# Optimization experiments

Hardware: AMD Instinct MI355X
Metric: run time of the kernel (lower is better)

The kernel has to match this reference:

```python
import jax, jax.numpy as jnp
import numpy as np

PNUM = 128
BATCH = 8192


def setup_inputs() -> dict:
    key = jax.random.key(0)
    k0, k1, k2 = jax.random.split(key, 3)
    return {
        "pred0": jax.random.normal(k0, (BATCH, PNUM, 2), dtype=jnp.float32),
        "pred1": jax.random.normal(k1, (BATCH, PNUM, 2), dtype=jnp.float32),
        "gt": jax.random.normal(k2, (BATCH, PNUM, 2), dtype=jnp.float32),
    }


def _smooth_l1(d):
    # F.smooth_l1_loss with default beta=1.0, reduction='none'
    a = jnp.abs(d)
    return jnp.where(a < 1.0, 0.5 * d * d, a - 0.5)


def _match_loss(pred, gt):
    # pred, gt: [B, pnum, 2]
    pnum = pred.shape[1]
    # cyclic index: idx[i, j] = (i + j) % pnum  (row i = gt rolled by i)
    idx = (jnp.arange(pnum)[:, None] + jnp.arange(pnum)[None, :]) % pnum
    gt_expand = gt[:, idx]                      # [B, pnum, pnum, 2]
    diff = pred[:, None, :, :] - gt_expand      # broadcast pred over shift dim i
    dis = _smooth_l1(diff).sum(-1).mean(axis=2)  # [B, pnum] mean over vertices j
    return jnp.min(dis, axis=1)                  # min over cyclic shift i -> [B]


def reference(pred0, pred1, gt):
    loss = _match_loss(pred0, gt).mean() + _match_loss(pred1, gt).mean()
    return loss / 2.0
```

## Files before the change

### kernel.cpp

```cpp
#include <hip/hip_runtime.h>

#define PNUM 128
#define BATCH 8192
#define WPB 4
#define GRID1 (BATCH / (2 * WPB))

typedef _Float16 h2 __attribute__((ext_vector_type(2)));
typedef _Float16 h4 __attribute__((ext_vector_type(4)));
typedef _Float16 h8 __attribute__((ext_vector_type(8)));

__device__ __forceinline__ h2 cvt2(float x, float y) {
    return __builtin_bit_cast(h2, __builtin_amdgcn_cvt_pkrtz(x, y));
}
__device__ __forceinline__ h4 cvt4(float4 v) {
    h2 a = cvt2(v.x, v.y), b = cvt2(v.z, v.w);
    return (h4){a.x, a.y, b.x, b.y};
}

__device__ __forceinline__ void unit(h2 p, h2 q, float& acc) {
    h2 d = p - q;
    h2 a = __builtin_bit_cast(h2, __builtin_bit_cast(unsigned, d) & 0x7fff7fffu);
    h2 m = __builtin_elementwise_min(a, (h2)(_Float16)1.0f);
    h2 t = __builtin_elementwise_fma(m, (h2)(_Float16)-0.5f, a);
    acc = __builtin_amdgcn_fdot2(m, t, acc, false);
}

__device__ __forceinline__ h2 lo2(h4 v) { return __builtin_shufflevector(v, v, 0, 1); }
__device__ __forceinline__ h2 hi2(h4 v) { return __builtin_shufflevector(v, v, 2, 3); }
__device__ __forceinline__ h4 lo4(h8 v) { return __builtin_shufflevector(v, v, 0, 1, 2, 3); }
__device__ __forceinline__ h4 hi4(h8 v) { return __builtin_shufflevector(v, v, 4, 5, 6, 7); }
__device__ __forceinline__ h2 el2(h8 v, int i) {
    return (h2){v[2 * i], v[2 * i + 1]};
}

__global__ __launch_bounds__(64 * WPB, 4) void match_fused(
        const float* __restrict__ pred0,
        const float* __restrict__ pred1,
        const float* __restrict__ gt,
        float* __restrict__ out) {
    __shared__ __align__(16) h4 ring [WPB][2][128];
    __shared__ __align__(16) h4 preds[WPB][2][2][64];

    const int t  = threadIdx.x;
    const int k  = t & 63;
    const int w  = __builtin_amdgcn_readfirstlane(t >> 6);
    const int h  = k >> 5;
    const int kk = k & 31;
    const int b  = 2 * (blockIdx.x * WPB + w) + h;

    h4* ring4 = ring[w][h];
    h4* q0 = preds[w][h][0];
    h4* q1 = preds[w][h][1];

    const float4* gv4 = (const float4*)(gt    + (size_t)b * (PNUM * 2));
    const float4* p0v = (const float4*)(pred0 + (size_t)b * (PNUM * 2));
    const float4* p1v = (const float4*)(pred1 + (size_t)b * (PNUM * 2));
    {
        h4 v = cvt4(gv4[kk]);      ring4[kk]      = v; ring4[kk + 64] = v;
        v    = cvt4(gv4[kk + 32]); ring4[kk + 32] = v; ring4[kk + 96] = v;
        q0[kk]      = cvt4(p0v[kk]);
        q0[kk + 32] = cvt4(p0v[kk + 32]);
        q1[kk]      = cvt4(p1v[kk]);
        q1[kk + 32] = cvt4(p1v[kk + 32]);
    }

    const h8* q0_8 = (const h8*)q0;
    const h8* q1_8 = (const h8*)q1;

    h8 wi = *(const h8*)&ring4[2 * kk];
    h4 w0 = lo4(wi), w1 = hi4(wi);

    float r00 = 0.f, r01 = 0.f, r02 = 0.f, r03 = 0.f;
    float r10 = 0.f, r11 = 0.f, r12 = 0.f, r13 = 0.f;

#pragma unroll 4
    for (int hh = 0; hh < 32; ++hh) {
        h8 n  = *(const h8*)&ring4[2 * kk + 2 * hh + 2];
        h8 P0 = q0_8[hh];
        h8 P1 = q1_8[hh];
        h4 w2 = lo4(n), w3 = hi4(n);

        h2 A0 = lo2(w0), A1 = hi2(w0), A2 = lo2(w1), A3 = hi2(w1);
        h2 A4 = lo2(w2), A5 = hi2(w2), A6 = lo2(w3);
        h2 p0a = el2(P0, 0), p0b = el2(P0, 1), p0c = el2(P0, 2), p0d = el2(P0, 3);
        h2 p1a = el2(P1, 0), p1b = el2(P1, 1), p1c = el2(P1, 2), p1d = el2(P1, 3);

        unit(p0a, A0, r00); unit(p0b, A1, r00); unit(p0c, A2, r00); unit(p0d, A3, r00);
        unit(p0a, A1, r01); unit(p0b, A2, r01); unit(p0c, A3, r01); unit(p0d, A4, r01);
        unit(p0a, A2, r02); unit(p0b, A3, r02); unit(p0c, A4, r02); unit(p0d, A5, r02);
        unit(p0a, A3, r03); unit(p0b, A4, r03); unit(p0c, A5, r03); unit(p0d, A6, r03);

        unit(p1a, A0, r10); unit(p1b, A1, r10); unit(p1c, A2, r10); unit(p1d, A3, r10);
        unit(p1a, A1, r11); unit(p1b, A2, r11); unit(p1c, A3, r11); unit(p1d, A4, r11);
        unit(p1a, A2, r12); unit(p1b, A3, r12); unit(p1c, A4, r12); unit(p1d, A5, r12);
        unit(p1a, A3, r13); unit(p1b, A4, r13); unit(p1c, A5, r13); unit(p1d, A6, r13);

        w0 = w2; w1 = w3;
    }

    float m0 = fminf(fminf(r00, r01), fminf(r02, r03));
    float m1 = fminf(fminf(r10, r11), fminf(r12, r13));
#pragma unroll
    for (int m = 16; m > 0; m >>= 1) {
        m0 = fminf(m0, __shfl_xor(m0, m, 64));
        m1 = fminf(m1, __shfl_xor(m1, m, 64));
    }
    float s = m0 + m1;
    s += __shfl_xor(s, 32, 64);

    __shared__ float bsum[WPB];
    if (k == 0) bsum[w] = s;
    __syncthreads();
    if (t == 0) {
        float blockpart = bsum[0] + bsum[1] + bsum[2] + bsum[3];
        atomicAdd(out, blockpart * (1.0f / (2.0f * BATCH * PNUM)));
    }
}

extern "C" void kernel_launch(void* const* d_in, const int* in_sizes, int n_in,
                              void* d_out, int out_size, void* d_ws, size_t ws_size,
                              hipStream_t stream) {
    const float* pred0 = (const float*)d_in[0];
    const float* pred1 = (const float*)d_in[1];
    const float* gt    = (const float*)d_in[2];
    float* out = (float*)d_out;

    (void)hipMemsetAsync(out, 0, sizeof(float), stream);
    match_fused<<<GRID1, 64 * WPB, 0, stream>>>(pred0, pred1, gt, out);
}
```

Measured before the change: 116.6 us.

## Split vertex loop across wave pairs and merge partial shift sums in LDS

```diff
diff --git a/kernel.cpp b/kernel.cpp
--- a/kernel.cpp
+++ b/kernel.cpp
@@ -2,8 +2,7 @@
 
 #define PNUM 128
 #define BATCH 8192
-#define WPB 4
-#define GRID1 (BATCH / (2 * WPB))
+#define GRID1 (BATCH / 4)
 
 typedef _Float16 h2 __attribute__((ext_vector_type(2)));
 typedef _Float16 h4 __attribute__((ext_vector_type(4)));
@@ -29,28 +28,30 @@
 __device__ __forceinline__ h2 hi2(h4 v) { return __builtin_shufflevector(v, v, 2, 3); }
 __device__ __forceinline__ h4 lo4(h8 v) { return __builtin_shufflevector(v, v, 0, 1, 2, 3); }
 __device__ __forceinline__ h4 hi4(h8 v) { return __builtin_shufflevector(v, v, 4, 5, 6, 7); }
-__device__ __forceinline__ h2 el2(h8 v, int i) {
-    return (h2){v[2 * i], v[2 * i + 1]};
-}
+__device__ __forceinline__ h2 el2(h8 v, int i) { return (h2){v[2 * i], v[2 * i + 1]}; }
 
-__global__ __launch_bounds__(64 * WPB, 4) void match_fused(
+__global__ __launch_bounds__(256, 8) void match_fused(
         const float* __restrict__ pred0,
         const float* __restrict__ pred1,
         const float* __restrict__ gt,
         float* __restrict__ out) {
-    __shared__ __align__(16) h4 ring [WPB][2][128];
-    __shared__ __align__(16) h4 preds[WPB][2][2][64];
+    __shared__ __align__(16) h4 ring [4][128];
+    __shared__ __align__(16) h4 preds[4][2][64];
+    __shared__ float part[2][8][64];
 
-    const int t  = threadIdx.x;
-    const int k  = t & 63;
-    const int w  = __builtin_amdgcn_readfirstlane(t >> 6);
-    const int h  = k >> 5;
-    const int kk = k & 31;
-    const int b  = 2 * (blockIdx.x * WPB + w) + h;
+    const int t    = threadIdx.x;
+    const int k    = t & 63;
+    const int w    = __builtin_amdgcn_readfirstlane(t >> 6);
+    const int pair = w >> 1;
+    const int sK   = w & 1;
+    const int h    = k >> 5;
+    const int kk   = k & 31;
+    const int bb   = 2 * pair + h;
+    const int b    = blockIdx.x * 4 + bb;
 
-    h4* ring4 = ring[w][h];
-    h4* q0 = preds[w][h][0];
-    h4* q1 = preds[w][h][1];
+    h4* ring4 = ring[bb];
+    h4* q0 = preds[bb][0];
+    h4* q1 = preds[bb][1];
 
     const float4* gv4 = (const float4*)(gt    + (size_t)b * (PNUM * 2));
     const float4* p0v = (const float4*)(pred0 + (size_t)b * (PNUM * 2));
@@ -67,14 +68,15 @@
     const h8* q0_8 = (const h8*)q0;
     const h8* q1_8 = (const h8*)q1;
 
-    h8 wi = *(const h8*)&ring4[2 * kk];
+    const int h0 = 16 * sK;
+    h8 wi = *(const h8*)&ring4[2 * kk + 32 * sK];
     h4 w0 = lo4(wi), w1 = hi4(wi);
 
     float r00 = 0.f, r01 = 0.f, r02 = 0.f, r03 = 0.f;
     float r10 = 0.f, r11 = 0.f, r12 = 0.f, r13 = 0.f;
 
 #pragma unroll 4
-    for (int hh = 0; hh < 32; ++hh) {
+    for (int hh = h0; hh < h0 + 16; ++hh) {
         h8 n  = *(const h8*)&ring4[2 * kk + 2 * hh + 2];
         h8 P0 = q0_8[hh];
         h8 P1 = q1_8[hh];
@@ -98,22 +100,35 @@
         w0 = w2; w1 = w3;
     }
 
-    float m0 = fminf(fminf(r00, r01), fminf(r02, r03));
-    float m1 = fminf(fminf(r10, r11), fminf(r12, r13));
+    if (sK) {
+        float* pp = &part[pair][0][k];
+        pp[0]       = r00; pp[64]      = r01; pp[2 * 64] = r02; pp[3 * 64] = r03;
+        pp[4 * 64]  = r10; pp[5 * 64]  = r11; pp[6 * 64] = r12; pp[7 * 64] = r13;
+    }
+    __syncthreads();
+
+    float s2 = 0.f;
+    if (!sK) {
+        const float* pp = &part[pair][0][k];
+        r00 += pp[0];       r01 += pp[64];      r02 += pp[2 * 64]; r03 += pp[3 * 64];
+        r10 += pp[4 * 64];  r11 += pp[5 * 64];  r12 += pp[6 * 64]; r13 += pp[7 * 64];
+
+        float m0 = fminf(fminf(r00, r01), fminf(r02, r03));
+        float m1 = fminf(fminf(r10, r11), fminf(r12, r13));
 #pragma unroll
-    for (int m = 16; m > 0; m >>= 1) {
-        m0 = fminf(m0, __shfl_xor(m0, m, 64));
-        m1 = fminf(m1, __shfl_xor(m1, m, 64));
+        for (int m = 16; m > 0; m >>= 1) {
+            m0 = fminf(m0, __shfl_xor(m0, m, 64));
+            m1 = fminf(m1, __shfl_xor(m1, m, 64));
+        }
+        s2 = m0 + m1;
+        s2 += __shfl_xor(s2, 32, 64);
     }
-    float s = m0 + m1;
-    s += __shfl_xor(s, 32, 64);
 
-    __shared__ float bsum[WPB];
-    if (k == 0) bsum[w] = s;
+    __shared__ float bsum[2];
+    if (!sK && k == 0) bsum[pair] = s2;
     __syncthreads();
     if (t == 0) {
-        float blockpart = bsum[0] + bsum[1] + bsum[2] + bsum[3];
-        atomicAdd(out, blockpart * (1.0f / (2.0f * BATCH * PNUM)));
+        atomicAdd(out, (bsum[0] + bsum[1]) * (1.0f / (2.0f * BATCH * PNUM)));
     }
 }
 
@@ -126,5 +141,5 @@
     float* out = (float*)d_out;
 
     (void)hipMemsetAsync(out, 0, sizeof(float), stream);
-    match_fused<<<GRID1, 64 * WPB, 0, stream>>>(pred0, pred1, gt, out);
+    match_fused<<<GRID1, 256, 0, stream>>>(pred0, pred1, gt, out);
 }
```

Result: slower. 119.7 us (+2.6%).
